# Kernel optimization log

Hardware: AMD Instinct MI355X
Metric: run time of the kernel (lower is better)

Reference implementation:

```python
import jax, jax.numpy as jnp
import numpy as np

H = 32          # total heads
K = 8           # active heads per token
D = 128         # head_dim = embed_dim // active_heads
E = 1024        # embed_dim
S = 1024        # seq_len
MAX_SEQ = 8192
BASE = 10000.0
SCALE = D ** -0.5
LB_W = 0.01
ENT_W = 0.01


def _rope(v, cos, sin):
    # v: (T, D); cos/sin: (T, D)
    v1, v2 = v[:, : D // 2], v[:, D // 2:]
    rot = jnp.concatenate([-v2, v1], axis=-1)
    return v * cos + rot * sin


def setup_inputs() -> dict:
    key = jax.random.key(0)
    ks = jax.random.split(key, 6)
    x = jax.random.normal(ks[0], (1, S, E), jnp.float32)
    Wq = jax.random.normal(ks[1], (E, H * D), jnp.float32) * 0.02
    Wk = jax.random.normal(ks[2], (E, H * D), jnp.float32) * 0.02
    Wv = jax.random.normal(ks[3], (E, H * D), jnp.float32) * 0.02
    Wr = jax.random.normal(ks[4], (E, H), jnp.float32) * 0.02
    Wo = jax.random.normal(ks[5], (K * D, E), jnp.float32) * 0.02
    head_counts = jnp.zeros((1, H), jnp.int32)
    return {"x": x, "Wq": Wq, "Wk": Wk, "Wv": Wv, "Wr": Wr, "Wo": Wo,
            "head_counts": head_counts}


def reference(x, Wq, Wk, Wv, Wr, Wo, head_counts):
    # ---- routing (eval mode: no gumbel noise) ----
    logits = x @ Wr                                   # (1, S, H)
    soft_probs = jax.nn.softmax(logits, axis=-1)
    top_logits, head_idx = jax.lax.top_k(logits, K)   # (1, S, K)
    head_w = jax.nn.softmax(top_logits, axis=-1)      # (1, S, K)

    # ---- aux loss ----
    primary = head_idx[..., 0]                        # (1, S)
    one_hot_p = jax.nn.one_hot(primary, H, dtype=jnp.float32)
    f = one_hot_p.mean(axis=1)                        # (1, H)
    p = soft_probs.mean(axis=1)                       # (1, H)
    balance = H * (f * p).sum(axis=-1).mean()
    entropy = -(soft_probs * jnp.log(soft_probs + 1e-8)).sum(axis=-1)
    entropy_loss = -entropy.mean()
    z_loss = (jax.nn.logsumexp(logits, axis=-1) ** 2).mean() * 0.01
    aux_loss = LB_W * balance + ENT_W * entropy_loss + z_loss

    # ---- projections + per-token gather of selected heads ----
    q_all = (x @ Wq).reshape(1, S, H, D)
    k_all = (x @ Wk).reshape(1, S, H, D)
    v_all = (x @ Wv).reshape(1, S, H, D)
    gidx = head_idx[..., None]                        # (1, S, K, 1)
    q = jnp.take_along_axis(q_all, gidx, axis=2)[0].reshape(S * K, D)
    k = jnp.take_along_axis(k_all, gidx, axis=2)[0].reshape(S * K, D)
    v = jnp.take_along_axis(v_all, gidx, axis=2)[0].reshape(S * K, D)

    heads_flat = head_idx[0].reshape(S * K)           # (T,)

    # rank of each dispatched token within its head (exclusive prefix count)
    oh = jax.nn.one_hot(heads_flat, H, dtype=jnp.int32)   # (T, H)
    excl = jnp.cumsum(oh, axis=0) - oh
    rank = jnp.take_along_axis(excl, heads_flat[:, None], axis=1)[:, 0]
    positions = rank + head_counts[0, heads_flat]
    positions = jnp.clip(positions, 0, MAX_SEQ - 1)

    # ---- per-head RoPE with per-head position counters ----
    inv_freq = 1.0 / (BASE ** (jnp.arange(0, D, 2, dtype=jnp.float32) / D))
    freqs = positions.astype(jnp.float32)[:, None] * inv_freq[None, :]
    emb = jnp.concatenate([freqs, freqs], axis=-1)    # (T, D)
    cos, sin = jnp.cos(emb), jnp.sin(emb)
    q = _rope(q, cos, sin)
    k = _rope(k, cos, sin)

    # ---- block-diagonal-causal attention (same head, earlier dispatch order) ----
    idx = jnp.arange(S * K)
    mask = (heads_flat[:, None] == heads_flat[None, :]) & (idx[None, :] <= idx[:, None])
    scores = (q @ k.T) * SCALE                        # (T, T)
    scores = jnp.where(mask, scores, jnp.float32(-1e30))
    attn = jax.nn.softmax(scores, axis=-1)
    out = attn @ v                                    # (T, D)

    # ---- combine with routing weights + output projection ----
    out = out.reshape(S, K, D) * head_w[0][..., None]
    out = out.reshape(S, K * D) @ Wo                  # (S, E)
    output = out[None]                                # (1, S, E)

    updated_counts = head_counts + oh.sum(axis=0)[None]
    return output, updated_counts, aux_loss
```

## Files before the change

### kernel.cpp

```cpp
#include <hip/hip_runtime.h>
#include <math.h>

#define S 1024
#define E 1024
#define H 32
#define KSEL 8
#define D 128
#define HD 4096
#define SK 8192
#define MAXL 1024
#define CAP 9216
#define ATTN_SCALE 0.08838834764831845f
#define SSTR 36
#define PSTR 40

#define NROUTERB 1024
#define NCONV 832
#define NTAB 512

typedef _Float16 half8 __attribute__((ext_vector_type(8)));
typedef _Float16 half4 __attribute__((ext_vector_type(4)));
typedef float floatx16 __attribute__((ext_vector_type(16)));
typedef float f4 __attribute__((ext_vector_type(4)));

#define GLOAD_LDS16(gsrc, ldst) \
    __builtin_amdgcn_global_load_lds( \
        (const __attribute__((address_space(1))) void*)(gsrc), \
        (__attribute__((address_space(3))) void*)(ldst), 16, 0, 0)


__device__ __forceinline__ void head_prefix(const int* __restrict__ hlen, int h,
                                            int lane, int& len, int& hb, int& lenp)
{
    int hl = (lane < 32) ? hlen[lane] : 0;
    int hp = (hl + 31) & ~31;
    int pref = hp;
    #pragma unroll
    for (int off = 1; off < 32; off <<= 1) {
        int t = __shfl_up(pref, off, 64);
        if (lane >= off) pref += t;
    }
    int excl = pref - hp;
    hb   = __shfl(excl, h, 64);
    len  = __shfl(hl, h, 64);
    lenp = (len + 31) & ~31;
}

__global__ __launch_bounds__(256) void router_conv_kernel(
    const float* __restrict__ x, const float* __restrict__ Wr,
    int* __restrict__ head_idx, float* __restrict__ head_w,
    float* __restrict__ pbuf, float* __restrict__ entz,
    _Float16* __restrict__ xh,
    const float* __restrict__ Wq, const float* __restrict__ Wk,
    const float* __restrict__ Wv, const float* __restrict__ Wo,
    _Float16* __restrict__ Wqkt, _Float16* __restrict__ Wot,
    float2* __restrict__ tab)
{
    int bid = blockIdx.x, tid = threadIdx.x;
    __shared__ __align__(16) char smem[128 * 128 * 2];
    if (bid >= NROUTERB + NCONV) {
        int base = (bid - NROUTERB - NCONV) * 1024;
        #pragma unroll
        for (int j = 0; j < 4; ++j) {
            int idx = base + j * 256 + tid;
            int p = idx >> 6, d2 = idx & 63;
            float inv = exp2f((float)d2 * -0.20762050f);
            float ang = (float)p * inv;
            float sn, cs;
            sincosf(ang, &sn, &cs);
            tab[idx] = make_float2(cs, sn);
        }
        return;
    }
    if (bid >= NROUTERB) {
        _Float16* tl = (_Float16*)smem;
        int cb = bid - NROUTERB;
        int z, rem;
        if (cb < 768) { z = cb >> 8; rem = cb & 255; }
        else          { z = 3;       rem = cb - 768; }
        const float* W = (z == 0) ? Wq : (z == 1) ? Wk : (z == 2) ? Wv : Wo;
        _Float16* T = (z < 3) ? (Wqkt + (size_t)z * HD * E) : Wot;
        int C = (z < 3) ? HD : 1024;
        int nc = C >> 7;
        int c0 = (rem % nc) * 128;
        int r0 = (rem / nc) * 128;
        #pragma unroll
        for (int p = 0; p < 16; ++p) {
            int idx = p * 256 + tid;
            int rr = idx >> 5, cg = (idx & 31) * 4;
            f4 v = *(const f4*)&W[(size_t)(r0 + rr) * C + c0 + cg];
            half4 o;
            o.x = (_Float16)v.x; o.y = (_Float16)v.y;
            o.z = (_Float16)v.z; o.w = (_Float16)v.w;
            int sc = cg ^ (((rr >> 3) & 7) << 2);
            *(half4*)&tl[rr * 128 + sc] = o;
        }
        __syncthreads();
        #pragma unroll
        for (int p = 0; p < 8; ++p) {
            int chunk = p * 256 + tid;
            int cc = chunk >> 4, ch = chunk & 15;
            int cidx = cc ^ ((ch & 7) << 2);
            half8 o;
            #pragma unroll
            for (int j = 0; j < 8; ++j)
                o[j] = tl[(ch * 8 + j) * 128 + cidx];
            *(half8*)&T[(size_t)(c0 + cc) * 1024 + r0 + ch * 8] = o;
        }
        return;
    }
    int s = bid;
    int w = tid >> 6, lane = tid & 63;
    int h = lane & 31;
    int seg = w * 2 + (lane >> 5);
    float* partial = (float*)smem;
    const float* xr = x + (size_t)s * E + seg * 128;
    const float* wr = Wr + (size_t)(seg * 128) * H + h;
    float a0 = 0.f, a1 = 0.f, a2 = 0.f, a3 = 0.f;
    #pragma unroll 4
    for (int e = 0; e < 128; e += 4) {
        a0 += xr[e]     * wr[e * H];
        a1 += xr[e + 1] * wr[(e + 1) * H];
        a2 += xr[e + 2] * wr[(e + 2) * H];
        a3 += xr[e + 3] * wr[(e + 3) * H];
    }
    float acc = (a0 + a1) + (a2 + a3);
    acc += __shfl_xor(acc, 32, 64);
    if (lane < 32) partial[w * 32 + h] = acc;
    __syncthreads();
    float logit = partial[h] + partial[32 + h] + partial[64 + h] + partial[96 + h];
    if (w == 0) {
        float m = logit;
        #pragma unroll
        for (int off = 16; off; off >>= 1) m = fmaxf(m, __shfl_xor(m, off, 64));
        float ex = expf(logit - m);
        float Z = ex;
        #pragma unroll
        for (int off = 16; off; off >>= 1) Z += __shfl_xor(Z, off, 64);
        float p = ex / Z;
        float es = p * logf(p + 1e-8f);
        #pragma unroll
        for (int off = 16; off; off >>= 1) es += __shfl_xor(es, off, 64);
        float lse = m + logf(Z);
        float lv = logit;
        float tv[KSEL]; int ti[KSEL];
        #pragma unroll
        for (int j = 0; j < KSEL; ++j) {
            float bv = lv; int bi = h;
            #pragma unroll
            for (int off = 16; off; off >>= 1) {
                float ov = __shfl_xor(bv, off, 64);
                int oi = __shfl_xor(bi, off, 64);
                if (ov > bv || (ov == bv && oi < bi)) { bv = ov; bi = oi; }
            }
            tv[j] = bv; ti[j] = bi;
            if (h == bi) lv = -INFINITY;
        }
        float Z2 = 0.f;
        #pragma unroll
        for (int j = 0; j < KSEL; ++j) Z2 += expf(tv[j] - tv[0]);
        if (lane < 32) pbuf[s * 32 + lane] = p;
        if (lane == 0) {
            entz[s * 2]     = es;
            entz[s * 2 + 1] = lse * lse;
            #pragma unroll
            for (int j = 0; j < KSEL; ++j) {
                head_idx[s * KSEL + j] = ti[j];
                head_w[s * KSEL + j]   = expf(tv[j] - tv[0]) / Z2;
            }
        }
    }
    {
        int e = tid * 4;
        f4 v = *(const f4*)&x[(size_t)s * E + e];
        half4 o;
        o.x = (_Float16)v.x; o.y = (_Float16)v.y; o.z = (_Float16)v.z; o.w = (_Float16)v.w;
        *(half4*)&xh[(size_t)s * E + e] = o;
    }
}

__global__ __launch_bounds__(256) void scan_aux_kernel(
    const int* __restrict__ head_idx, const int* __restrict__ head_counts,
    int* __restrict__ order, int* __restrict__ hlen, float* __restrict__ out_counts,
    const float* __restrict__ pbuf, const float* __restrict__ entz,
    float* __restrict__ out_aux)
{
    int bid = blockIdx.x, tid = threadIdx.x;
    if (bid == H) {
        int hh = tid & 31, grp = tid >> 5;
        __shared__ float red[256], red2[256];
        __shared__ float psum[32];
        __shared__ int hist[32];
        if (tid < 32) hist[tid] = 0;
        float ps = 0.f;
        for (int s = grp; s < S; s += 8) ps += pbuf[s * 32 + hh];
        red[tid] = ps;
        float es = 0.f, zs = 0.f;
        for (int s = tid; s < S; s += 256) { es += entz[s * 2]; zs += entz[s * 2 + 1]; }
        red2[tid] = es;
        __syncthreads();
        if (grp == 0) {
            float v = 0.f;
            #pragma unroll
            for (int j = 0; j < 8; ++j) v += red[j * 32 + hh];
            psum[hh] = v;
        }
        __syncthreads();
        red[tid] = zs;
        for (int s = tid; s < S; s += 256)
            atomicAdd(&hist[head_idx[s * KSEL]], 1);
        __syncthreads();
        for (int stp = 128; stp; stp >>= 1) {
            if (tid < stp) { red[tid] += red[tid + stp]; red2[tid] += red2[tid + stp]; }
            __syncthreads();
        }
        if (tid == 0) {
            float bal = 0.f;
            for (int j = 0; j < H; ++j)
                bal += ((float)hist[j] / (float)S) * (psum[j] / (float)S);
            bal *= (float)H;
            float ent_loss = red2[0] / (float)S;
            float z = red[0] / (float)S * 0.01f;
            out_aux[0] = 0.01f * bal + 0.01f * ent_loss + z;
        }
        return;
    }
    int h = bid;
    int wave = tid >> 6, lane = tid & 63;
    __shared__ int wtot[4][4];
    int base = 0;
    int hc = head_counts[h];
    int v0 = head_idx[tid],       v1 = head_idx[256 + tid];
    int v2 = head_idx[512 + tid], v3 = head_idx[768 + tid];
    unsigned long long lt = (1ull << lane) - 1ull;
    for (int c0 = 0; c0 < SK; c0 += 1024) {
        int n0 = 0, n1 = 0, n2 = 0, n3 = 0;
        if (c0 + 1024 < SK) {
            n0 = head_idx[c0 + 1024 + tid]; n1 = head_idx[c0 + 1280 + tid];
            n2 = head_idx[c0 + 1536 + tid]; n3 = head_idx[c0 + 1792 + tid];
        }
        bool p0 = (v0 == h), p1 = (v1 == h), p2 = (v2 == h), p3 = (v3 == h);
        unsigned long long m0 = __ballot(p0), m1 = __ballot(p1);
        unsigned long long m2 = __ballot(p2), m3 = __ballot(p3);
        int w0 = __popcll(m0 & lt), w1 = __popcll(m1 & lt);
        int w2 = __popcll(m2 & lt), w3 = __popcll(m3 & lt);
        if (lane == 0) {
            wtot[0][wave] = __popcll(m0); wtot[1][wave] = __popcll(m1);
            wtot[2][wave] = __popcll(m2); wtot[3][wave] = __popcll(m3);
        }
        __syncthreads();
        int pw[4], T[4];
        #pragma unroll
        for (int i = 0; i < 4; ++i) {
            int pre = 0, tot = 0;
            #pragma unroll
            for (int w = 0; w < 4; ++w) {
                int tv = wtot[i][w];
                if (w < wave) pre += tv;
                tot += tv;
            }
            pw[i] = pre; T[i] = tot;
        }
        if (p0) order[h * MAXL + base + pw[0] + w0] = c0 + tid;
        if (p1) order[h * MAXL + base + T[0] + pw[1] + w1] = c0 + 256 + tid;
        if (p2) order[h * MAXL + base + T[0] + T[1] + pw[2] + w2] = c0 + 512 + tid;
        if (p3) order[h * MAXL + base + T[0] + T[1] + T[2] + pw[3] + w3] = c0 + 768 + tid;
        base += T[0] + T[1] + T[2] + T[3];
        __syncthreads();
        v0 = n0; v1 = n1; v2 = n2; v3 = n3;
    }
    if (tid == 0) {
        hlen[h] = base;
        out_counts[h] = (float)(hc + base);
    }
}

__global__ __launch_bounds__(256) void qkv_mfma(
    const _Float16* __restrict__ xh, const _Float16* __restrict__ Wt,
    const int* __restrict__ order, const int* __restrict__ hlen,
    const int* __restrict__ head_counts, const float2* __restrict__ tab,
    _Float16* __restrict__ qh, _Float16* __restrict__ kh, _Float16* __restrict__ vT)
{
    int xid = blockIdx.x;
    int qkv = xid >> 5, h = xid & 31;
    int rt = blockIdx.y;
    int tid = threadIdx.x, wave = tid >> 6, lane = tid & 63;
    int len, hb, lenp;
    head_prefix(hlen, h, lane, len, hb, lenp);
    int row0 = rt * 64;
    if (row0 >= len) return;
    int wm = wave >> 1, wn = wave & 1;
    int l32 = lane & 31, g = lane >> 5;

    __shared__ _Float16 Bs[2][128 * 64];

    int arow_g = row0 + wm * 32 + l32;
    int tok = (arow_g < len) ? (order[h * MAXL + arow_g] >> 3) : 0;
    const _Float16* aptr = xh + (size_t)tok * E;
    const _Float16* Wb = Wt + (size_t)((qkv * H + h) * D) * E;

    auto stageB = [&](int buf, int k0) {
        #pragma unroll
        for (int it = 0; it < 4; ++it) {
            int f = it * 256 + tid;
            int row = f >> 3, c = f & 7;
            int sc = c ^ (row & 7);
            const _Float16* src = Wb + (size_t)row * E + k0 + sc * 8;
            GLOAD_LDS16(src, &Bs[buf][f * 8]);
        }
    };

    floatx16 acc[2] = {};
    half8 a_cur[4], a_nxt[4];
    #pragma unroll
    for (int ks = 0; ks < 4; ++ks)
        a_cur[ks] = *(const half8*)(aptr + ks * 16 + g * 8);

    auto compute = [&](int buf, half8* a) {
        #pragma unroll
        for (int ks = 0; ks < 4; ++ks) {
            int wchunk = ks * 2 + g;
            #pragma unroll
            for (int nf = 0; nf < 2; ++nf) {
                int brow = wn * 64 + nf * 32 + l32;
                half8 bf = *(const half8*)&Bs[buf][brow * 64 + (wchunk ^ (brow & 7)) * 8];
                acc[nf] = __builtin_amdgcn_mfma_f32_32x32x16_f16(a[ks], bf, acc[nf], 0, 0, 0);
            }
        }
    };

    stageB(0, 0);
    __syncthreads();
    int buf = 0;
    for (int k0 = 64; k0 < E; k0 += 64) {
        stageB(buf ^ 1, k0);
        #pragma unroll
        for (int ks = 0; ks < 4; ++ks)
            a_nxt[ks] = *(const half8*)(aptr + k0 + ks * 16 + g * 8);
        compute(buf, a_cur);
        __syncthreads();
        buf ^= 1;
        #pragma unroll
        for (int ks = 0; ks < 4; ++ks) a_cur[ks] = a_nxt[ks];
    }
    compute(buf, a_cur);

    if (qkv < 2) {
        _Float16* dst = (qkv == 0) ? qh : kh;
        float* scr = (float*)&Bs[0][0];
        __syncthreads();
        #pragma unroll
        for (int nf = 0; nf < 2; ++nf) {
            int col = wn * 64 + nf * 32 + l32;
            #pragma unroll
            for (int reg = 0; reg < 16; ++reg) {
                int rl = wm * 32 + (reg & 3) + 8 * (reg >> 2) + 4 * g;
                scr[rl * 128 + col] = acc[nf][reg];
            }
        }
        __syncthreads();
        int hc = head_counts[h];
        #pragma unroll
        for (int pass = 0; pass < 16; ++pass) {
            int idx = pass * 256 + tid;
            int r = idx >> 6, d2 = idx & 63;
            int slot = row0 + r;
            if (slot < len) {
                float v1 = scr[r * 128 + d2], v2 = scr[r * 128 + 64 + d2];
                int p = slot + hc;
                p = p < 0 ? 0 : (p > 8191 ? 8191 : p);
                float2 tt = tab[p * 64 + d2];
                size_t tb = (size_t)(hb + (slot & ~31)) * D;
                int sl5 = slot & 31;
                int c0 = d2 >> 3, e0 = d2 & 7;
                dst[tb + (size_t)(c0 * 32 + sl5) * 8 + e0]       = (_Float16)(v1 * tt.x - v2 * tt.y);
                dst[tb + (size_t)((c0 + 8) * 32 + sl5) * 8 + e0] = (_Float16)(v2 * tt.x + v1 * tt.y);
            }
        }
    } else {
        #pragma unroll
        for (int nf = 0; nf < 2; ++nf) {
            int col = wn * 64 + nf * 32 + l32;
            #pragma unroll
            for (int q4 = 0; q4 < 4; ++q4) {
                int slot0 = row0 + wm * 32 + 8 * q4 + 4 * g;
                size_t tb = (size_t)(hb + (slot0 & ~31)) * D;
                int sc = (slot0 & 31) >> 3;
                _Float16* vp = vT + tb + (size_t)(sc * 128 + col) * 8 + (slot0 & 7);
                if (slot0 + 3 < len) {
                    half4 o;
                    o.x = (_Float16)acc[nf][q4 * 4 + 0];
                    o.y = (_Float16)acc[nf][q4 * 4 + 1];
                    o.z = (_Float16)acc[nf][q4 * 4 + 2];
                    o.w = (_Float16)acc[nf][q4 * 4 + 3];
                    *(half4*)vp = o;
                } else {
                    #pragma unroll
                    for (int r2 = 0; r2 < 4; ++r2) {
                        int sl = slot0 + r2;
                        if (sl < len) vp[r2] = (_Float16)acc[nf][q4 * 4 + r2];
                        else if (sl < lenp) vp[r2] = (_Float16)0.f;
                    }
                }
            }
        }
    }
}

__global__ __launch_bounds__(128) void attn_mfma(
    const _Float16* __restrict__ qh, const _Float16* __restrict__ kh,
    const _Float16* __restrict__ vT,
    const int* __restrict__ order, const int* __restrict__ hlen,
    const float* __restrict__ head_w, _Float16* __restrict__ ao)
{
    int h = blockIdx.x & 31;
    int qt = 31 - (int)(blockIdx.x >> 5);
    int tid = threadIdx.x;
    int w = tid >> 6, lane = tid & 63;
    int len, hb, lenp;
    head_prefix(hlen, h, lane, len, hb, lenp);
    int row0 = qt * 32;
    if (row0 >= len) return;
    int l32 = lane & 31, g = lane >> 5;
    int srow = lane >> 1, shalf = lane & 1;

    __shared__ float Sld[2][32 * SSTR];
    __shared__ _Float16 Pld[2][32 * PSTR];
    __shared__ float alphaLd[2][32];
    __shared__ float mlLd[32][4];
    __shared__ float facLd[32][3];
    __shared__ int flatLd[32];
    __shared__ float Obuf[32][128];

    if (tid < 32) {
        int r = row0 + tid;
        flatLd[tid] = (r < len) ? order[h * MAXL + r] : -1;
    }

    const _Float16* qtile = qh + (size_t)(hb + row0) * D;
    half8 qf[8];
    #pragma unroll
    for (int t = 0; t < 8; ++t)
        qf[t] = *(const half8*)(qtile + (size_t)((t * 2 + g) * 32 + l32) * 8);

    floatx16 O[4] = {};
    float m_run = -INFINITY, l_run = 0.f;

    if (w <= qt) {
        half8 kf[8], kfn[8], vv[8];
        {
            const _Float16* ktile = kh + (size_t)(hb + w * 32) * D;
            #pragma unroll
            for (int t = 0; t < 8; ++t)
                kf[t] = *(const half8*)(ktile + (size_t)((t * 2 + g) * 32 + l32) * 8);
        }
        for (int kt = w; kt <= qt; kt += 2) {
            int col0 = kt * 32;
            floatx16 Sc = {};
            #pragma unroll
            for (int t = 0; t < 8; ++t)
                Sc = __builtin_amdgcn_mfma_f32_32x32x16_f16(qf[t], kf[t], Sc, 0, 0, 0);
            {
                const _Float16* vtile = vT + (size_t)(hb + col0) * D;
                #pragma unroll
                for (int nt = 0; nt < 4; ++nt) {
                    vv[nt * 2]     = *(const half8*)(vtile + (size_t)(g * 128 + nt * 32 + l32) * 8);
                    vv[nt * 2 + 1] = *(const half8*)(vtile + (size_t)((2 + g) * 128 + nt * 32 + l32) * 8);
                }
            }
            if (kt + 2 <= qt) {
                const _Float16* ktile = kh + (size_t)(hb + col0 + 64) * D;
                #pragma unroll
                for (int t = 0; t < 8; ++t)
                    kfn[t] = *(const half8*)(ktile + (size_t)((t * 2 + g) * 32 + l32) * 8);
            }
            bool diag = (kt == qt);
            #pragma unroll
            for (int reg = 0; reg < 16; ++reg) {
                int row = (reg & 3) + 8 * (reg >> 2) + 4 * g;
                float s = Sc[reg] * ATTN_SCALE;
                if (diag && l32 > row) s = -1e30f;
                Sld[w][row * SSTR + l32] = s;
            }
            __builtin_amdgcn_wave_barrier();
            const float* sp = &Sld[w][srow * SSTR + shalf * 16];
            float va[16];
            *(f4*)(va)      = *(const f4*)(sp);
            *(f4*)(va + 4)  = *(const f4*)(sp + 4);
            *(f4*)(va + 8)  = *(const f4*)(sp + 8);
            *(f4*)(va + 12) = *(const f4*)(sp + 12);
            float mt_ = va[0];
            #pragma unroll
            for (int j = 1; j < 16; ++j) mt_ = fmaxf(mt_, va[j]);
            mt_ = fmaxf(mt_, __shfl_xor(mt_, 1, 64));
            float m_new = fmaxf(m_run, mt_);
            float alpha = __expf(m_run - m_new);
            float p[16], tsum = 0.f;
            #pragma unroll
            for (int j = 0; j < 16; ++j) { p[j] = __expf(va[j] - m_new); tsum += p[j]; }
            tsum += __shfl_xor(tsum, 1, 64);
            l_run = l_run * alpha + tsum;
            m_run = m_new;
            half8 ph0, ph1;
            #pragma unroll
            for (int j = 0; j < 8; ++j) { ph0[j] = (_Float16)p[j]; ph1[j] = (_Float16)p[j + 8]; }
            *(half8*)&Pld[w][srow * PSTR + shalf * 16]     = ph0;
            *(half8*)&Pld[w][srow * PSTR + shalf * 16 + 8] = ph1;
            if (shalf == 0) alphaLd[w][srow] = alpha;
            __builtin_amdgcn_wave_barrier();
            f4 al[4];
            #pragma unroll
            for (int qq = 0; qq < 4; ++qq) al[qq] = *(const f4*)&alphaLd[w][4 * g + 8 * qq];
            #pragma unroll
            for (int reg = 0; reg < 16; ++reg) {
                float av = al[reg >> 2][reg & 3];
                O[0][reg] *= av; O[1][reg] *= av; O[2][reg] *= av; O[3][reg] *= av;
            }
            half8 pf0 = *(const half8*)&Pld[w][l32 * PSTR + g * 8];
            half8 pf1 = *(const half8*)&Pld[w][l32 * PSTR + 16 + g * 8];
            #pragma unroll
            for (int nt = 0; nt < 4; ++nt) {
                O[nt] = __builtin_amdgcn_mfma_f32_32x32x16_f16(pf0, vv[nt * 2],     O[nt], 0, 0, 0);
                O[nt] = __builtin_amdgcn_mfma_f32_32x32x16_f16(pf1, vv[nt * 2 + 1], O[nt], 0, 0, 0);
            }
            __builtin_amdgcn_wave_barrier();
            #pragma unroll
            for (int t = 0; t < 8; ++t) kf[t] = kfn[t];
        }
    }
    if (shalf == 0) { mlLd[srow][w * 2] = m_run; mlLd[srow][w * 2 + 1] = l_run; }
    __syncthreads();
    if (tid < 32) {
        float m0 = mlLd[tid][0], l0 = mlLd[tid][1];
        float m1 = mlLd[tid][2], l1 = mlLd[tid][3];
        float ms = fmaxf(m0, m1);
        float f0 = __expf(m0 - ms), f1 = __expf(m1 - ms);
        float lt = f0 * l0 + f1 * l1;
        int flat = flatLd[tid];
        float hw = (flat >= 0) ? head_w[flat] : 0.f;
        facLd[tid][0] = f1;
        facLd[tid][1] = hw / lt;
        facLd[tid][2] = f0;
    }
    __syncthreads();
    if (w == 1) {
        #pragma unroll
        for (int nt = 0; nt < 4; ++nt) {
            int col = nt * 32 + l32;
            #pragma unroll
            for (int reg = 0; reg < 16; ++reg) {
                int row = (reg & 3) + 8 * (reg >> 2) + 4 * g;
                Obuf[row][col] = O[nt][reg] * facLd[row][0];
            }
        }
    }
    __syncthreads();
    if (w == 0) {
        #pragma unroll
        for (int nt = 0; nt < 4; ++nt) {
            int col = nt * 32 + l32;
            #pragma unroll
            for (int reg = 0; reg < 16; ++reg) {
                int row = (reg & 3) + 8 * (reg >> 2) + 4 * g;
                int flat = flatLd[row];
                if (flat >= 0) {
                    float val = (O[nt][reg] * facLd[row][2] + Obuf[row][col]) * facLd[row][1];
                    ao[(size_t)flat * D + col] = (_Float16)val;
                }
            }
        }
    }
}

__global__ __launch_bounds__(256) void out_mfma(
    const _Float16* __restrict__ A, const _Float16* __restrict__ Bt,
    float* __restrict__ C)
{
    int n0 = blockIdx.x * 64, m0 = blockIdx.y * 64;
    int tid = threadIdx.x, wave = tid >> 6, lane = tid & 63;
    int wm = wave >> 1, wn = wave & 1;
    int l32 = lane & 31, g = lane >> 5;

    __shared__ _Float16 Bs[2][64 * 64];

    const _Float16* aptr = A + (size_t)(m0 + wm * 32 + l32) * 1024;

    auto stageB = [&](int buf, int k0) {
        #pragma unroll
        for (int it = 0; it < 2; ++it) {
            int f = it * 256 + tid;
            int row = f >> 3, c = f & 7;
            int sc = c ^ (row & 7);
            GLOAD_LDS16(Bt + (size_t)(n0 + row) * 1024 + k0 + sc * 8, &Bs[buf][f * 8]);
        }
    };

    floatx16 acc = {};
    int brow = wn * 32 + l32;
    half8 a_cur[4], a_nxt[4];
    #pragma unroll
    for (int ks = 0; ks < 4; ++ks)
        a_cur[ks] = *(const half8*)(aptr + ks * 16 + g * 8);

    auto compute = [&](int buf, half8* a) {
        #pragma unroll
        for (int ks = 0; ks < 4; ++ks) {
            int wchunk = ks * 2 + g;
            half8 bf = *(const half8*)&Bs[buf][brow * 64 + (wchunk ^ (brow & 7)) * 8];
            acc = __builtin_amdgcn_mfma_f32_32x32x16_f16(a[ks], bf, acc, 0, 0, 0);
        }
    };

    stageB(0, 0);
    __syncthreads();
    int buf = 0;
    for (int k0 = 64; k0 < 1024; k0 += 64) {
        stageB(buf ^ 1, k0);
        #pragma unroll
        for (int ks = 0; ks < 4; ++ks)
            a_nxt[ks] = *(const half8*)(aptr + k0 + ks * 16 + g * 8);
        compute(buf, a_cur);
        __syncthreads();
        buf ^= 1;
        #pragma unroll
        for (int ks = 0; ks < 4; ++ks) a_cur[ks] = a_nxt[ks];
    }
    compute(buf, a_cur);

    int col = n0 + wn * 32 + l32;
    #pragma unroll
    for (int reg = 0; reg < 16; ++reg) {
        int row = m0 + wm * 32 + (reg & 3) + 8 * (reg >> 2) + 4 * g;
        C[(size_t)row * 1024 + col] = acc[reg];
    }
}

extern "C" void kernel_launch(void* const* d_in, const int* in_sizes, int n_in,
                              void* d_out, int out_size, void* d_ws, size_t ws_size,
                              hipStream_t stream)
{
    const float* x  = (const float*)d_in[0];
    const float* Wq = (const float*)d_in[1];
    const float* Wk = (const float*)d_in[2];
    const float* Wv = (const float*)d_in[3];
    const float* Wr = (const float*)d_in[4];
    const float* Wo = (const float*)d_in[5];
    const int* head_counts = (const int*)d_in[6];
    float* out = (float*)d_out;

    float* head_w = (float*)d_ws;
    float* pbuf   = head_w + SK;
    float* entz   = pbuf + S * 32;
    int* head_idx = (int*)(entz + S * 2);
    int* order    = head_idx + SK;
    int* hlen     = order + H * MAXL;
    _Float16* xh   = (_Float16*)(hlen + 64);
    _Float16* aoh  = xh + (size_t)S * E;
    _Float16* Wqkt = aoh + (size_t)SK * D;
    _Float16* Wot  = Wqkt + (size_t)3 * HD * E;
    _Float16* qh   = Wot + (size_t)1024 * 1024;
    _Float16* kh   = qh + (size_t)CAP * D;
    _Float16* vT   = kh + (size_t)CAP * D;
    float2* tab    = (float2*)(vT + (size_t)CAP * D);

    router_conv_kernel<<<NROUTERB + NCONV + NTAB, 256, 0, stream>>>(
        x, Wr, head_idx, head_w, pbuf, entz, xh, Wq, Wk, Wv, Wo, Wqkt, Wot, tab);
    scan_aux_kernel<<<33, 256, 0, stream>>>(head_idx, head_counts, order, hlen,
                                            out + (size_t)S * E, pbuf, entz,
                                            out + (size_t)S * E + H);
    qkv_mfma<<<dim3(96, 16), 256, 0, stream>>>(xh, Wqkt, order, hlen, head_counts, tab,
                                               qh, kh, vT);
    attn_mfma<<<H * 32, 128, 0, stream>>>(qh, kh, vT, order, hlen, head_w, aoh);
    out_mfma<<<dim3(16, 16), 256, 0, stream>>>(aoh, Wot, out);
}
```

Baseline: 206.9 us.

## Widen scan chunks, vectorize RoPE epilogue stores, double out_mfma M tile

```diff
diff --git a/kernel.cpp b/kernel.cpp
--- a/kernel.cpp
+++ b/kernel.cpp
@@ -227,47 +227,49 @@
     }
     int h = bid;
     int wave = tid >> 6, lane = tid & 63;
-    __shared__ int wtot[4][4];
+    __shared__ int wtot[8][4];
     int base = 0;
     int hc = head_counts[h];
-    int v0 = head_idx[tid],       v1 = head_idx[256 + tid];
-    int v2 = head_idx[512 + tid], v3 = head_idx[768 + tid];
+    int v[8], n[8];
+    #pragma unroll
+    for (int j = 0; j < 8; ++j) v[j] = head_idx[j * 256 + tid];
     unsigned long long lt = (1ull << lane) - 1ull;
-    for (int c0 = 0; c0 < SK; c0 += 1024) {
-        int n0 = 0, n1 = 0, n2 = 0, n3 = 0;
-        if (c0 + 1024 < SK) {
-            n0 = head_idx[c0 + 1024 + tid]; n1 = head_idx[c0 + 1280 + tid];
-            n2 = head_idx[c0 + 1536 + tid]; n3 = head_idx[c0 + 1792 + tid];
-        }
-        bool p0 = (v0 == h), p1 = (v1 == h), p2 = (v2 == h), p3 = (v3 == h);
-        unsigned long long m0 = __ballot(p0), m1 = __ballot(p1);
-        unsigned long long m2 = __ballot(p2), m3 = __ballot(p3);
-        int w0 = __popcll(m0 & lt), w1 = __popcll(m1 & lt);
-        int w2 = __popcll(m2 & lt), w3 = __popcll(m3 & lt);
-        if (lane == 0) {
-            wtot[0][wave] = __popcll(m0); wtot[1][wave] = __popcll(m1);
-            wtot[2][wave] = __popcll(m2); wtot[3][wave] = __popcll(m3);
-        }
-        __syncthreads();
-        int pw[4], T[4];
-        #pragma unroll
-        for (int i = 0; i < 4; ++i) {
-            int pre = 0, tot = 0;
+    for (int c0 = 0; c0 < SK; c0 += 2048) {
+        #pragma unroll
+        for (int j = 0; j < 8; ++j)
+            n[j] = (c0 + 2048 < SK) ? head_idx[c0 + 2048 + j * 256 + tid] : 0;
+        bool p[8];
+        int wi[8];
+        #pragma unroll
+        for (int j = 0; j < 8; ++j) {
+            p[j] = (v[j] == h);
+            unsigned long long m = __ballot(p[j]);
+            wi[j] = __popcll(m & lt);
+            if (lane == 0) wtot[j][wave] = __popcll(m);
+        }
+        __syncthreads();
+        int pre[8], T[8];
+        #pragma unroll
+        for (int i = 0; i < 8; ++i) {
+            int pr = 0, tot = 0;
             #pragma unroll
             for (int w = 0; w < 4; ++w) {
                 int tv = wtot[i][w];
-                if (w < wave) pre += tv;
+                if (w < wave) pr += tv;
                 tot += tv;
             }
-            pw[i] = pre; T[i] = tot;
-        }
-        if (p0) order[h * MAXL + base + pw[0] + w0] = c0 + tid;
-        if (p1) order[h * MAXL + base + T[0] + pw[1] + w1] = c0 + 256 + tid;
-        if (p2) order[h * MAXL + base + T[0] + T[1] + pw[2] + w2] = c0 + 512 + tid;
-        if (p3) order[h * MAXL + base + T[0] + T[1] + T[2] + pw[3] + w3] = c0 + 768 + tid;
-        base += T[0] + T[1] + T[2] + T[3];
-        __syncthreads();
-        v0 = n0; v1 = n1; v2 = n2; v3 = n3;
+            pre[i] = pr; T[i] = tot;
+        }
+        int run = base;
+        #pragma unroll
+        for (int j = 0; j < 8; ++j) {
+            if (p[j]) order[h * MAXL + run + pre[j] + wi[j]] = c0 + j * 256 + tid;
+            run += T[j];
+        }
+        base = run;
+        __syncthreads();
+        #pragma unroll
+        for (int j = 0; j < 8; ++j) v[j] = n[j];
     }
     if (tid == 0) {
         hlen[h] = base;
@@ -361,20 +363,30 @@
         __syncthreads();
         int hc = head_counts[h];
         #pragma unroll
-        for (int pass = 0; pass < 16; ++pass) {
-            int idx = pass * 256 + tid;
-            int r = idx >> 6, d2 = idx & 63;
+        for (int pass = 0; pass < 2; ++pass) {
+            int item = pass * 256 + tid;
+            int r = item >> 3;
+            int c0 = item & 7;
             int slot = row0 + r;
             if (slot < len) {
-                float v1 = scr[r * 128 + d2], v2 = scr[r * 128 + 64 + d2];
                 int p = slot + hc;
                 p = p < 0 ? 0 : (p > 8191 ? 8191 : p);
-                float2 tt = tab[p * 64 + d2];
+                float vv1[8], vv2[8];
+                *(f4*)(vv1)     = *(const f4*)&scr[r * 128 + c0 * 8];
+                *(f4*)(vv1 + 4) = *(const f4*)&scr[r * 128 + c0 * 8 + 4];
+                *(f4*)(vv2)     = *(const f4*)&scr[r * 128 + 64 + c0 * 8];
+                *(f4*)(vv2 + 4) = *(const f4*)&scr[r * 128 + 64 + c0 * 8 + 4];
+                half8 o1, o2;
+                #pragma unroll
+                for (int j = 0; j < 8; ++j) {
+                    float2 tt = tab[p * 64 + c0 * 8 + j];
+                    o1[j] = (_Float16)(vv1[j] * tt.x - vv2[j] * tt.y);
+                    o2[j] = (_Float16)(vv2[j] * tt.x + vv1[j] * tt.y);
+                }
                 size_t tb = (size_t)(hb + (slot & ~31)) * D;
                 int sl5 = slot & 31;
-                int c0 = d2 >> 3, e0 = d2 & 7;
-                dst[tb + (size_t)(c0 * 32 + sl5) * 8 + e0]       = (_Float16)(v1 * tt.x - v2 * tt.y);
-                dst[tb + (size_t)((c0 + 8) * 32 + sl5) * 8 + e0] = (_Float16)(v2 * tt.x + v1 * tt.y);
+                *(half8*)&dst[tb + (size_t)(c0 * 32 + sl5) * 8]       = o1;
+                *(half8*)&dst[tb + (size_t)((c0 + 8) * 32 + sl5) * 8] = o2;
             }
         }
     } else {
@@ -576,14 +588,15 @@
     const _Float16* __restrict__ A, const _Float16* __restrict__ Bt,
     float* __restrict__ C)
 {
-    int n0 = blockIdx.x * 64, m0 = blockIdx.y * 64;
+    int n0 = blockIdx.x * 64, m0 = blockIdx.y * 128;
     int tid = threadIdx.x, wave = tid >> 6, lane = tid & 63;
     int wm = wave >> 1, wn = wave & 1;
     int l32 = lane & 31, g = lane >> 5;
 
     __shared__ _Float16 Bs[2][64 * 64];
 
-    const _Float16* aptr = A + (size_t)(m0 + wm * 32 + l32) * 1024;
+    const _Float16* aptr0 = A + (size_t)(m0 + wm * 32 + l32) * 1024;
+    const _Float16* aptr1 = A + (size_t)(m0 + 64 + wm * 32 + l32) * 1024;
 
     auto stageB = [&](int buf, int k0) {
         #pragma unroll
@@ -595,19 +608,22 @@
         }
     };
 
-    floatx16 acc = {};
+    floatx16 acc0 = {}, acc1 = {};
     int brow = wn * 32 + l32;
-    half8 a_cur[4], a_nxt[4];
+    half8 a_cur[2][4], a_nxt[2][4];
     #pragma unroll
-    for (int ks = 0; ks < 4; ++ks)
-        a_cur[ks] = *(const half8*)(aptr + ks * 16 + g * 8);
-
-    auto compute = [&](int buf, half8* a) {
+    for (int ks = 0; ks < 4; ++ks) {
+        a_cur[0][ks] = *(const half8*)(aptr0 + ks * 16 + g * 8);
+        a_cur[1][ks] = *(const half8*)(aptr1 + ks * 16 + g * 8);
+    }
+
+    auto compute = [&](int buf, half8 a[2][4]) {
         #pragma unroll
         for (int ks = 0; ks < 4; ++ks) {
             int wchunk = ks * 2 + g;
             half8 bf = *(const half8*)&Bs[buf][brow * 64 + (wchunk ^ (brow & 7)) * 8];
-            acc = __builtin_amdgcn_mfma_f32_32x32x16_f16(a[ks], bf, acc, 0, 0, 0);
+            acc0 = __builtin_amdgcn_mfma_f32_32x32x16_f16(a[0][ks], bf, acc0, 0, 0, 0);
+            acc1 = __builtin_amdgcn_mfma_f32_32x32x16_f16(a[1][ks], bf, acc1, 0, 0, 0);
         }
     };
 
@@ -617,21 +633,27 @@
     for (int k0 = 64; k0 < 1024; k0 += 64) {
         stageB(buf ^ 1, k0);
         #pragma unroll
-        for (int ks = 0; ks < 4; ++ks)
-            a_nxt[ks] = *(const half8*)(aptr + k0 + ks * 16 + g * 8);
+        for (int ks = 0; ks < 4; ++ks) {
+            a_nxt[0][ks] = *(const half8*)(aptr0 + k0 + ks * 16 + g * 8);
+            a_nxt[1][ks] = *(const half8*)(aptr1 + k0 + ks * 16 + g * 8);
+        }
         compute(buf, a_cur);
         __syncthreads();
         buf ^= 1;
         #pragma unroll
-        for (int ks = 0; ks < 4; ++ks) a_cur[ks] = a_nxt[ks];
+        for (int ks = 0; ks < 4; ++ks) {
+            a_cur[0][ks] = a_nxt[0][ks];
+            a_cur[1][ks] = a_nxt[1][ks];
+        }
     }
     compute(buf, a_cur);
 
     int col = n0 + wn * 32 + l32;
     #pragma unroll
     for (int reg = 0; reg < 16; ++reg) {
-        int row = m0 + wm * 32 + (reg & 3) + 8 * (reg >> 2) + 4 * g;
-        C[(size_t)row * 1024 + col] = acc[reg];
+        int rbase = wm * 32 + (reg & 3) + 8 * (reg >> 2) + 4 * g;
+        C[(size_t)(m0 + rbase) * 1024 + col]      = acc0[reg];
+        C[(size_t)(m0 + 64 + rbase) * 1024 + col] = acc1[reg];
     }
 }
 
@@ -671,5 +693,5 @@
     qkv_mfma<<<dim3(96, 16), 256, 0, stream>>>(xh, Wqkt, order, hlen, head_counts, tab,
                                                qh, kh, vT);
     attn_mfma<<<H * 32, 128, 0, stream>>>(qh, kh, vT, order, hlen, head_w, aoh);
-    out_mfma<<<dim3(16, 16), 256, 0, stream>>>(aoh, Wot, out);
+    out_mfma<<<dim3(16, 8), 256, 0, stream>>>(aoh, Wot, out);
 }
```

Result: no change. 208.2 us (+0.6%).
